# Kernel tuning notes

Hardware: AMD Instinct MI355X
Metric: run time of the kernel (lower is better)

Reference implementation:

```python
import jax, jax.numpy as jnp
import numpy as np


def setup_inputs() -> dict:
    key = jax.random.key(0)
    k1, k2 = jax.random.split(key)
    B, N, M = 8, 8192, 8192
    points1 = jax.random.normal(k1, (B, N, 2), dtype=jnp.float32)
    points2 = jax.random.normal(k2, (B, M, 2), dtype=jnp.float32)
    return {"points1": points1, "points2": points2}


def reference(points1, points2):
    # points1: [B, N, 2], points2: [B, M, 2]
    # Squared pairwise distances via |a|^2 + |b|^2 - 2 a.b  -> [B, N, M]
    p1_sq = jnp.sum(points1 * points1, axis=-1)  # [B, N]
    p2_sq = jnp.sum(points2 * points2, axis=-1)  # [B, M]
    cross = jnp.einsum("bnd,bmd->bnm", points1, points2)  # [B, N, M]
    sqdist = p1_sq[:, :, None] + p2_sq[:, None, :] - 2.0 * cross
    dist1 = jnp.min(sqdist, axis=2)  # [B, N]: NN of each p1 point in p2
    dist2 = jnp.min(sqdist, axis=1)  # [B, M]: NN of each p2 point in p1
    cost = jnp.mean(dist1, axis=-1) + jnp.mean(dist2, axis=-1)  # [B]
    return jnp.sum(cost)
```

## Files before the change

kernel.cpp:

```cpp
#include <hip/hip_runtime.h>


#define BATCH 8
#define NPTS  8192
#define TPB   256
#define IPT   8
#define PPB   (TPB * IPT)
#define TILES (NPTS / PPB)
#define S     32
#define JCH   (NPTS / S)

__device__ inline float min3f(float a, float b, float c) {
    float d;
    asm("v_min3_f32 %0, %1, %2, %3" : "=v"(d) : "v"(a), "v"(b), "v"(c));
    return d;
}

__global__ __launch_bounds__(TPB, 8)
void chamfer_partial(const float* __restrict__ p1, const float* __restrict__ p2,
                     float* __restrict__ partial ,
                     float* __restrict__ out_to_zero) {
    __shared__ float4 q[JCH];

    if (blockIdx.x == 0 && threadIdx.x == 0) *out_to_zero = 0.0f;

    int blk   = blockIdx.x;
    int split = blk & (S - 1);      blk >>= 5;
    int tile  = blk & (TILES - 1);  blk >>= 2;
    int b     = blk & (BATCH - 1);  blk >>= 3;
    int dir   = blk;

    const float2* a  = (const float2*)(dir ? p2 : p1) + (size_t)b * NPTS;
    const float2* bp = (const float2*)(dir ? p1 : p2) + (size_t)b * NPTS + split * JCH;

    int t = threadIdx.x;

    for (int j = t; j < JCH; j += TPB) {
        float2 v = bp[j];
        q[j] = make_float4(v.x, v.y, fmaf(v.x, v.x, v.y * v.y), 0.0f);
    }

    int pt_base = tile * PPB;
    float xp[IPT], yp[IPT], m[IPT];
#pragma unroll
    for (int k = 0; k < IPT; ++k) {
        float2 v = a[pt_base + k * TPB + t];
        xp[k] = -2.0f * v.x;
        yp[k] = -2.0f * v.y;
        m[k]  = 3.0e38f;
    }

    __syncthreads();

    for (int j = 0; j < JCH; j += 4) {
        float4 q0 = q[j + 0], q1 = q[j + 1], q2 = q[j + 2], q3 = q[j + 3];
#pragma unroll
        for (int k = 0; k < IPT; ++k) {
            float t0 = fmaf(yp[k], q0.y, fmaf(xp[k], q0.x, q0.z));
            float t1 = fmaf(yp[k], q1.y, fmaf(xp[k], q1.x, q1.z));
            float t2 = fmaf(yp[k], q2.y, fmaf(xp[k], q2.x, q2.z));
            float t3 = fmaf(yp[k], q3.y, fmaf(xp[k], q3.x, q3.z));
            m[k] = min3f(m[k], t0, t1);
            m[k] = min3f(m[k], t2, t3);
        }
    }

    float* outp = partial + ((size_t)((dir * BATCH + b) * S + split)) * NPTS + pt_base;
#pragma unroll
    for (int k = 0; k < IPT; ++k)
        outp[k * TPB + t] = m[k];
}

__global__ __launch_bounds__(TPB)
void chamfer_reduce(const float* __restrict__ p1, const float* __restrict__ p2,
                    const float* __restrict__ partial, float* __restrict__ out) {
    int gid   = blockIdx.x * TPB + threadIdx.x;
    int point = gid & (NPTS - 1);
    int rest  = gid >> 13;
    int b     = rest & (BATCH - 1);
    int dir   = rest >> 3;

    const float* base = partial + ((size_t)(dir * BATCH + b) * S) * NPTS + point;
    float m = base[0];
#pragma unroll
    for (int s = 1; s < S; ++s)
        m = fminf(m, base[(size_t)s * NPTS]);

    float2 v = ((const float2*)(dir ? p2 : p1))[(size_t)b * NPTS + point];
    float d = m + fmaf(v.x, v.x, v.y * v.y);

#pragma unroll
    for (int off = 32; off > 0; off >>= 1)
        d += __shfl_down(d, off, 64);

    __shared__ float wsum[TPB / 64];
    int lane = threadIdx.x & 63;
    int w    = threadIdx.x >> 6;
    if (lane == 0) wsum[w] = d;
    __syncthreads();
    if (threadIdx.x == 0) {
        float ssum = wsum[0] + wsum[1] + wsum[2] + wsum[3];
        atomicAdd(out, ssum * (1.0f / NPTS));
    }
}

extern "C" void kernel_launch(void* const* d_in, const int* in_sizes, int n_in,
                              void* d_out, int out_size, void* d_ws, size_t ws_size,
                              hipStream_t stream) {
    const float* p1 = (const float*)d_in[0];
    const float* p2 = (const float*)d_in[1];
    float* out      = (float*)d_out;
    float* partial  = (float*)d_ws;

    chamfer_partial<<<2 * BATCH * TILES * S, TPB, 0, stream>>>(p1, p2, partial, out);
    chamfer_reduce<<<2 * BATCH * NPTS / TPB, TPB, 0, stream>>>(p1, p2, partial, out);
}
```

Measured before the change: 125.8 us.

## Use packed FP32 FMA with SoA shared layout and deterministic final reduction

Stores the second point set in shared memory as separate x, y and squared-norm arrays so that pairs of neighbouring points load as packed float2 operands, and computes two distance terms per instruction with v_pk_fma_f32. The main loop now processes eight reference points per iteration. The launch bounds hint drops from 8 to 4 blocks per SIMD to leave more registers for the duplicated packed operands. The atomicAdd into the output is replaced by per-block sums plus a third single-block kernel. This removes the output zeroing and atomics at the cost of an extra launch.

New measurement: 115.9 us. -7.9%, faster.

```diff
diff --git a/kernel.cpp b/kernel.cpp
--- a/kernel.cpp
+++ b/kernel.cpp
@@ -9,6 +9,7 @@
 #define TILES (NPTS / PPB)
 #define S     32
 #define JCH   (NPTS / S)
+#define PARTN (2 * BATCH * S * NPTS)
 
 __device__ inline float min3f(float a, float b, float c) {
     float d;
@@ -16,13 +17,18 @@
     return d;
 }
 
-__global__ __launch_bounds__(TPB, 8)
+__device__ inline float2 pkfma(float2 a, float2 b, float2 c) {
+    float2 d;
+    asm("v_pk_fma_f32 %0, %1, %2, %3" : "=v"(d) : "v"(a), "v"(b), "v"(c));
+    return d;
+}
+
+__global__ __launch_bounds__(TPB, 4)
 void chamfer_partial(const float* __restrict__ p1, const float* __restrict__ p2,
-                     float* __restrict__ partial ,
-                     float* __restrict__ out_to_zero) {
-    __shared__ float4 q[JCH];
-
-    if (blockIdx.x == 0 && threadIdx.x == 0) *out_to_zero = 0.0f;
+                     float* __restrict__ partial ) {
+    __shared__ __align__(16) float qx[JCH];
+    __shared__ __align__(16) float qy[JCH];
+    __shared__ __align__(16) float qz[JCH];
 
     int blk   = blockIdx.x;
     int split = blk & (S - 1);      blk >>= 5;
@@ -35,33 +41,49 @@
 
     int t = threadIdx.x;
 
-    for (int j = t; j < JCH; j += TPB) {
-        float2 v = bp[j];
-        q[j] = make_float4(v.x, v.y, fmaf(v.x, v.x, v.y * v.y), 0.0f);
+    {
+        float2 v = bp[t];
+        qx[t] = v.x;
+        qy[t] = v.y;
+        qz[t] = fmaf(v.x, v.x, v.y * v.y);
     }
 
     int pt_base = tile * PPB;
-    float xp[IPT], yp[IPT], m[IPT];
+    float2 xp2[IPT], yp2[IPT];
+    float m[IPT];
 #pragma unroll
     for (int k = 0; k < IPT; ++k) {
         float2 v = a[pt_base + k * TPB + t];
-        xp[k] = -2.0f * v.x;
-        yp[k] = -2.0f * v.y;
-        m[k]  = 3.0e38f;
+        xp2[k] = make_float2(-2.0f * v.x, -2.0f * v.x);
+        yp2[k] = make_float2(-2.0f * v.y, -2.0f * v.y);
+        m[k]   = 3.0e38f;
     }
 
     __syncthreads();
 
-    for (int j = 0; j < JCH; j += 4) {
-        float4 q0 = q[j + 0], q1 = q[j + 1], q2 = q[j + 2], q3 = q[j + 3];
+    for (int j = 0; j < JCH; j += 8) {
+        float4 x03 = *(const float4*)&qx[j];
+        float4 x47 = *(const float4*)&qx[j + 4];
+        float4 y03 = *(const float4*)&qy[j];
+        float4 y47 = *(const float4*)&qy[j + 4];
+        float4 z03 = *(const float4*)&qz[j];
+        float4 z47 = *(const float4*)&qz[j + 4];
+        float2 x01 = make_float2(x03.x, x03.y), x23 = make_float2(x03.z, x03.w);
+        float2 x45 = make_float2(x47.x, x47.y), x67 = make_float2(x47.z, x47.w);
+        float2 y01 = make_float2(y03.x, y03.y), y23 = make_float2(y03.z, y03.w);
+        float2 y45 = make_float2(y47.x, y47.y), y67 = make_float2(y47.z, y47.w);
+        float2 z01 = make_float2(z03.x, z03.y), z23 = make_float2(z03.z, z03.w);
+        float2 z45 = make_float2(z47.x, z47.y), z67 = make_float2(z47.z, z47.w);
 #pragma unroll
         for (int k = 0; k < IPT; ++k) {
-            float t0 = fmaf(yp[k], q0.y, fmaf(xp[k], q0.x, q0.z));
-            float t1 = fmaf(yp[k], q1.y, fmaf(xp[k], q1.x, q1.z));
-            float t2 = fmaf(yp[k], q2.y, fmaf(xp[k], q2.x, q2.z));
-            float t3 = fmaf(yp[k], q3.y, fmaf(xp[k], q3.x, q3.z));
-            m[k] = min3f(m[k], t0, t1);
-            m[k] = min3f(m[k], t2, t3);
+            float2 a01 = pkfma(yp2[k], y01, pkfma(xp2[k], x01, z01));
+            float2 a23 = pkfma(yp2[k], y23, pkfma(xp2[k], x23, z23));
+            float2 a45 = pkfma(yp2[k], y45, pkfma(xp2[k], x45, z45));
+            float2 a67 = pkfma(yp2[k], y67, pkfma(xp2[k], x67, z67));
+            m[k] = min3f(m[k], a01.x, a01.y);
+            m[k] = min3f(m[k], a23.x, a23.y);
+            m[k] = min3f(m[k], a45.x, a45.y);
+            m[k] = min3f(m[k], a67.x, a67.y);
         }
     }
 
@@ -73,7 +95,7 @@
 
 __global__ __launch_bounds__(TPB)
 void chamfer_reduce(const float* __restrict__ p1, const float* __restrict__ p2,
-                    const float* __restrict__ partial, float* __restrict__ out) {
+                    const float* __restrict__ partial, float* __restrict__ bsum) {
     int gid   = blockIdx.x * TPB + threadIdx.x;
     int point = gid & (NPTS - 1);
     int rest  = gid >> 13;
@@ -98,10 +120,26 @@
     int w    = threadIdx.x >> 6;
     if (lane == 0) wsum[w] = d;
     __syncthreads();
-    if (threadIdx.x == 0) {
-        float ssum = wsum[0] + wsum[1] + wsum[2] + wsum[3];
-        atomicAdd(out, ssum * (1.0f / NPTS));
-    }
+    if (threadIdx.x == 0)
+        bsum[blockIdx.x] = wsum[0] + wsum[1] + wsum[2] + wsum[3];
+}
+
+__global__ __launch_bounds__(TPB)
+void chamfer_final(const float* __restrict__ bsum, float* __restrict__ out) {
+    int t = threadIdx.x;
+    float s = bsum[t] + bsum[t + TPB];
+
+#pragma unroll
+    for (int off = 32; off > 0; off >>= 1)
+        s += __shfl_down(s, off, 64);
+
+    __shared__ float wsum[TPB / 64];
+    int lane = t & 63;
+    int w    = t >> 6;
+    if (lane == 0) wsum[w] = s;
+    __syncthreads();
+    if (t == 0)
+        *out = (wsum[0] + wsum[1] + wsum[2] + wsum[3]) * (1.0f / NPTS);
 }
 
 extern "C" void kernel_launch(void* const* d_in, const int* in_sizes, int n_in,
@@ -111,7 +149,9 @@
     const float* p2 = (const float*)d_in[1];
     float* out      = (float*)d_out;
     float* partial  = (float*)d_ws;
+    float* bsum     = partial + PARTN;
 
-    chamfer_partial<<<2 * BATCH * TILES * S, TPB, 0, stream>>>(p1, p2, partial, out);
-    chamfer_reduce<<<2 * BATCH * NPTS / TPB, TPB, 0, stream>>>(p1, p2, partial, out);
+    chamfer_partial<<<2 * BATCH * TILES * S, TPB, 0, stream>>>(p1, p2, partial);
+    chamfer_reduce<<<2 * BATCH * NPTS / TPB, TPB, 0, stream>>>(p1, p2, partial, bsum);
+    chamfer_final<<<1, TPB, 0, stream>>>(bsum, out);
 }
```
